# Performance work log

Measured on AMD Instinct MI355X. Metric: run time of the kernel, lower is better.

The kernel has to match this reference:

```python
import jax, jax.numpy as jnp
import numpy as np

E = 768; H = 64; W = 64; K = 3; PAD = 1
CH = [30, 100, 150, 220, 268]


def _conv3x3(x, w, b):
    out = jax.lax.conv_general_dilated(x, w, (1, 1), ((PAD, PAD), (PAD, PAD)),
                                       dimension_numbers=('NCHW', 'OIHW', 'NCHW'))
    return out + b[None, :, None, None]


def _deform_conv(x, offset, mask, w, b):
    # modulated deform_conv2d, group=1, stride=1, dil=1, pad=1 (torchvision semantics)
    N, C, Hh, Ww = x.shape
    KK = K * K
    off = offset.reshape(N, KK, 2, Hh, Ww)  # [...,0]=dy, [...,1]=dx per kernel tap
    ky = jnp.repeat(jnp.arange(K), K).astype(x.dtype)
    kx = jnp.tile(jnp.arange(K), K).astype(x.dtype)
    hg = jnp.arange(Hh, dtype=x.dtype)[None, None, :, None]
    wg = jnp.arange(Ww, dtype=x.dtype)[None, None, None, :]
    py = hg - PAD + ky[None, :, None, None] + off[:, :, 0]  # [N,9,H,W]
    px = wg - PAD + kx[None, :, None, None] + off[:, :, 1]
    y0 = jnp.floor(py); x0 = jnp.floor(px)
    xf = x.reshape(N, C, Hh * Ww)

    def gather(yi, xi):
        valid = ((yi >= 0) & (yi <= Hh - 1) & (xi >= 0) & (xi <= Ww - 1)).astype(x.dtype)
        yc = jnp.clip(yi, 0, Hh - 1).astype(jnp.int32)
        xc = jnp.clip(xi, 0, Ww - 1).astype(jnp.int32)
        idx = (yc * Ww + xc).reshape(N, 1, KK * Hh * Ww)
        g = jnp.take_along_axis(xf, idx, axis=2).reshape(N, C, KK, Hh, Ww)
        return g * valid[:, None]

    wy1 = py - y0; wx1 = px - x0; wy0 = 1.0 - wy1; wx0 = 1.0 - wx1
    samp = (gather(y0, x0) * (wy0 * wx0)[:, None]
            + gather(y0, x0 + 1) * (wy0 * wx1)[:, None]
            + gather(y0 + 1, x0) * (wy1 * wx0)[:, None]
            + gather(y0 + 1, x0 + 1) * (wy1 * wx1)[:, None])
    samp = samp * mask[:, None]  # modulation
    out = jnp.einsum('nckhw,ock->nohw', samp, w.reshape(w.shape[0], C, KK))
    return out + b[None, :, None, None]


def _block(x, conv_w, conv_b, off_w, off_b, msk_w, msk_b, bn_g, bn_b):
    # DefConv2d.forward: conv -> offset/mask linears -> deform conv -> BN(train stats) -> relu
    N, C, Hh, Ww = x.shape
    om = _conv3x3(x, conv_w, conv_b)
    om_hwc = om.transpose(0, 2, 3, 1)
    offset = (om_hwc @ off_w.T + off_b).transpose(0, 3, 1, 2)  # [N,18,H,W]
    mask = jax.nn.softmax(om_hwc @ msk_w.T + msk_b, axis=-1)   # [N,H,W,9]
    mask = mask.reshape(N, K * K, Hh, Ww)  # raw reshape, exactly as torch .reshape (no permute)
    out = _deform_conv(x, offset, mask, conv_w, conv_b)
    mu = out.mean(axis=(0, 2, 3), keepdims=True)
    var = out.var(axis=(0, 2, 3), keepdims=True)
    out = (out - mu) / jnp.sqrt(var + 1e-5) * bn_g[None, :, None, None] + bn_b[None, :, None, None]
    return jax.nn.relu(out)


def _cam(x, chq_w, chv_w, chz_w, ln_g, ln_b, spq_w, spv_w):
    xin = x
    N, C, Hh, Ww = x.shape  # N must be 1 (matches torch reshapes)
    # channel attention
    wv = jnp.einsum('nchw,oc->nohw', x, chv_w).reshape(C // 2, Hh * Ww)
    wq = jax.nn.softmax(jnp.einsum('nchw,oc->nohw', x, chq_w).reshape(Hh * Ww))
    wz = chz_w @ (wv @ wq)  # [C]
    wz = (wz - wz.mean()) / jnp.sqrt(wz.var() + 1e-5) * ln_g + ln_b
    x = jax.nn.sigmoid(wz)[None, :, None, None] * x
    # spatial attention
    wq = jax.nn.softmax(jnp.einsum('nchw,oc->nohw', x, spq_w).max(axis=(2, 3)).reshape(C // 2))
    wv = jnp.einsum('nchw,oc->nohw', x, spv_w).reshape(C // 2, Hh * Ww)
    wz = jax.nn.sigmoid(wq @ wv).reshape(1, 1, Hh, Ww)
    return wz * x + xin


def _forward(x1, x2, x3, x4, x5, conv_w, conv_b, off_w, off_b, msk_w, msk_b, bn_g, bn_b,
             chq_w, chv_w, chz_w, ln_g, ln_b, spq_w, spv_w,
             w1, w2, w3a, w3b, w4a, w4b, w5a, w5b, norm_g, norm_b):
    xper = [t.transpose(0, 3, 1, 2) for t in (x1, x2, x3, x4, x5)]
    blk = lambda t: _block(t, conv_w, conv_b, off_w, off_b, msk_w, msk_b, bn_g, bn_b)
    c1 = lambda t, w: jnp.einsum('nchw,oc->nohw', t, w)
    o1 = c1(blk(xper[0]), w1)
    o2 = c1(blk(xper[1]), w2)
    o3 = c1(blk(xper[2]), w3a) + c1(xper[2], w3b)
    o4 = c1(blk(xper[3]), w4a) + c1(xper[3], w4b)
    o5 = c1(blk(xper[4]), w5a) + c1(xper[4], w5b)
    out = jnp.concatenate((o1, o2, o3, o4, o5), axis=1)  # sum(CH)=768 channels
    out = _cam(out, chq_w, chv_w, chz_w, ln_g, ln_b, spq_w, spv_w)
    out = (out + xper[4]).transpose(0, 2, 3, 1)
    mu = out.mean(-1, keepdims=True)
    var = out.var(-1, keepdims=True)
    return (out - mu) / jnp.sqrt(var + 1e-5) * norm_g + norm_b


def setup_inputs() -> dict:
    key = jax.random.key(0)
    ks = iter(jax.random.split(key, 40))
    rnd = lambda shape, s=0.05: jax.random.normal(next(ks), shape, dtype=jnp.float32) * s
    d = {}
    for i in range(5):
        d[f'x{i+1}'] = jax.random.normal(next(ks), (1, H, W, E), dtype=jnp.float32)
    d['conv_w'] = rnd((E, E, 3, 3), 0.02)
    d['conv_b'] = jnp.zeros((E,), jnp.float32)
    d['off_w'] = rnd((2 * 9, E), 0.01); d['off_b'] = jnp.zeros((18,), jnp.float32)
    d['msk_w'] = rnd((9, E), 0.01); d['msk_b'] = jnp.zeros((9,), jnp.float32)
    d['bn_g'] = jnp.ones((E,), jnp.float32); d['bn_b'] = jnp.zeros((E,), jnp.float32)
    C = sum(CH)  # 768
    d['chq_w'] = rnd((1, C)); d['chv_w'] = rnd((C // 2, C)); d['chz_w'] = rnd((C, C // 2))
    d['ln_g'] = jnp.ones((C,), jnp.float32); d['ln_b'] = jnp.zeros((C,), jnp.float32)
    d['spq_w'] = rnd((C // 2, C)); d['spv_w'] = rnd((C // 2, C))
    d['w1'] = rnd((CH[0], E)); d['w2'] = rnd((CH[1], E))
    d['w3a'] = rnd((CH[2], E)); d['w3b'] = rnd((CH[2], E))
    d['w4a'] = rnd((CH[3], E)); d['w4b'] = rnd((CH[3], E))
    d['w5a'] = rnd((CH[4], E)); d['w5b'] = rnd((CH[4], E))
    d['norm_g'] = jnp.ones((E,), jnp.float32); d['norm_b'] = jnp.zeros((E,), jnp.float32)
    return d


def reference(x1, x2, x3, x4, x5, conv_w, conv_b, off_w, off_b, msk_w, msk_b, bn_g, bn_b,
              chq_w, chv_w, chz_w, ln_g, ln_b, spq_w, spv_w,
              w1, w2, w3a, w3b, w4a, w4b, w5a, w5b, norm_g, norm_b):
    return _forward(x1, x2, x3, x4, x5, conv_w, conv_b, off_w, off_b, msk_w, msk_b, bn_g, bn_b,
                    chq_w, chv_w, chz_w, ln_g, ln_b, spq_w, spv_w,
                    w1, w2, w3a, w3b, w4a, w4b, w5a, w5b, norm_g, norm_b)
```

## Files before the change

kernel.cpp:

```cpp
#include <hip/hip_runtime.h>
#include <cstdint>
#include <cstddef>

#define HW 4096
#define CDIM 768
#define PPIX 4356

typedef unsigned short u16;
typedef __attribute__((ext_vector_type(8))) short short8;
typedef __attribute__((ext_vector_type(4))) float f32x4;

__device__ __forceinline__ float bf2f(u16 u) { return __uint_as_float(((unsigned)u) << 16); }
__device__ __forceinline__ u16 f2bf(float f) {
    unsigned u = __float_as_uint(f);
    unsigned r = (u + 0x7fffu + ((u >> 16) & 1u)) >> 16;
    return (u16)r;
}
__device__ __forceinline__ float lof(unsigned u) { return __uint_as_float(u << 16); }
__device__ __forceinline__ float hif(unsigned u) { return __uint_as_float(u & 0xffff0000u); }
__device__ __forceinline__ int swz(int r) { return ((r >> 1) ^ (r >> 3)) & 3; }

__device__ __forceinline__ void gl16(const u16* g, u16* l) {
    __builtin_amdgcn_global_load_lds(
        (const __attribute__((address_space(1))) unsigned int*)g,
        (__attribute__((address_space(3))) unsigned int*)l, 16, 0, 0);
}

enum GMode { G_CONV = 0, G_PROJ = 2, G_SPAT = 3 };

struct ProjP {
    const u16* b1[5];
    const u16* b2[5];
    int ch[5];
    int choff[5];
};

template <int MODE>
__launch_bounds__(256, 4)
__global__ void k_gemm128(const u16* __restrict__ xpad, const u16* __restrict__ blkA,
                          const u16* __restrict__ Wt, const float* __restrict__ bias,
                          u16* __restrict__ outb, float* __restrict__ outf, ProjP pp) {
    const int z = blockIdx.z;
    const int m0 = blockIdx.x * 128;
    const int n0 = blockIdx.y * 128;

    int Nrows, ntap, choff = 0, ldo = CDIM;
    const u16 *Az = nullptr, *Ac = nullptr, *B1 = nullptr, *B2 = nullptr;
    if constexpr (MODE == G_CONV) {
        Az = xpad + (size_t)z * PPIX * CDIM; B1 = Wt; Nrows = 768; ntap = 9;
    } else if constexpr (MODE == G_PROJ) {
        Ac = blkA + (size_t)z * HW * CDIM;
        Az = xpad + (size_t)z * PPIX * CDIM;
        B1 = pp.b1[z]; B2 = pp.b2[z];
        Nrows = pp.ch[z]; choff = pp.choff[z];
        ntap = B2 ? 2 : 1;
        if (n0 >= Nrows) return;
    } else {
        Ac = blkA; B1 = Wt; Nrows = 384; ntap = 1; ldo = 384;
    }

    __shared__ __align__(16) u16 As[128 * 32];
    __shared__ __align__(16) u16 Bs[128 * 32];

    const int t = threadIdx.x;
    const int lane = t & 63;
    const int wid = t >> 6;
    const int wrow = (wid >> 1) * 64, wcol = (wid & 1) * 64;
    const int lm = lane & 15;
    const int quad = lane >> 4;

    const int rS = t >> 2;
    const int cs0 = (t & 3) ^ swz(rS);
    const int cs1 = (t & 3) ^ swz(64 + rS);

    const u16 *a0 = nullptr, *a1 = nullptr, *a0x = nullptr, *a1x = nullptr;
    if constexpr (MODE == G_CONV) {
        int p0 = m0 + rS, p1 = m0 + 64 + rS;
        a0 = Az + (size_t)(((p0 >> 6)) * 66 + (p0 & 63)) * CDIM + cs0 * 8;
        a1 = Az + (size_t)(((p1 >> 6)) * 66 + (p1 & 63)) * CDIM + cs1 * 8;
    } else if constexpr (MODE == G_PROJ) {
        int p0 = m0 + rS, p1 = m0 + 64 + rS;
        a0 = Ac + (size_t)p0 * CDIM + cs0 * 8;
        a1 = Ac + (size_t)p1 * CDIM + cs1 * 8;
        a0x = Az + (size_t)(((p0 >> 6) + 1) * 66 + (p0 & 63) + 1) * CDIM + cs0 * 8;
        a1x = Az + (size_t)(((p1 >> 6) + 1) * 66 + (p1 & 63) + 1) * CDIM + cs1 * 8;
    } else {
        a0 = Ac + (size_t)(m0 + rS) * CDIM + cs0 * 8;
        a1 = Ac + (size_t)(m0 + 64 + rS) * CDIM + cs1 * 8;
    }
    const u16* b0 = B1 + (size_t)(n0 + rS) * CDIM + cs0 * 8;
    const u16* b1p = B1 + (size_t)(n0 + 64 + rS) * CDIM + cs1 * 8;
    const u16 *c0 = nullptr, *c1 = nullptr;
    if constexpr (MODE == G_PROJ) {
        if (B2) {
            c0 = B2 + (size_t)(n0 + rS) * CDIM + cs0 * 8;
            c1 = B2 + (size_t)(n0 + 64 + rS) * CDIM + cs1 * 8;
        }
    }

    u16* dA0 = &As[(0 * 4 + wid) * 512];
    u16* dA1 = &As[(1 * 4 + wid) * 512];
    u16* dB0 = &Bs[(0 * 4 + wid) * 512];
    u16* dB1 = &Bs[(1 * 4 + wid) * 512];

    f32x4 acc[4][4];
#pragma unroll
    for (int i = 0; i < 4; i++)
#pragma unroll
        for (int j = 0; j < 4; j++) acc[i][j] = (f32x4){0.f, 0.f, 0.f, 0.f};

    const int totS = ntap * 24;
    int tap = 0;
    int tA = 0, tB = 0, kO = 0;

    for (int s = 0; s < totS; ++s) {
        __syncthreads();
        if constexpr (MODE == G_CONV) {
            gl16(a0 + tA + kO, dA0);
            gl16(a1 + tA + kO, dA1);
            gl16(b0 + tB + kO, dB0);
            gl16(b1p + tB + kO, dB1);
        } else if constexpr (MODE == G_PROJ) {
            if (tap == 0) {
                gl16(a0 + kO, dA0);
                gl16(a1 + kO, dA1);
                gl16(b0 + kO, dB0);
                gl16(b1p + kO, dB1);
            } else {
                gl16(a0x + kO, dA0);
                gl16(a1x + kO, dA1);
                gl16(c0 + kO, dB0);
                gl16(c1 + kO, dB1);
            }
        } else {
            gl16(a0 + kO, dA0);
            gl16(a1 + kO, dA1);
            gl16(b0 + kO, dB0);
            gl16(b1p + kO, dB1);
        }
        __syncthreads();
        short8 af[4], bf[4];
#pragma unroll
        for (int i = 0; i < 4; i++) {
            int rr = wrow + i * 16 + lm;
            af[i] = *(const short8*)&As[rr * 32 + ((quad ^ swz(rr)) * 8)];
        }
#pragma unroll
        for (int j = 0; j < 4; j++) {
            int rr = wcol + j * 16 + lm;
            bf[j] = *(const short8*)&Bs[rr * 32 + ((quad ^ swz(rr)) * 8)];
        }
#pragma unroll
        for (int i = 0; i < 4; i++)
#pragma unroll
            for (int j = 0; j < 4; j++)
                acc[i][j] = __builtin_amdgcn_mfma_f32_16x16x32_bf16(af[i], bf[j], acc[i][j], 0, 0, 0);
        tap++;
        if constexpr (MODE == G_CONV) {
            tA += (tap == 3 || tap == 6) ? 64 * CDIM : CDIM;
            tB += CDIM * CDIM;
            if (tap == 9) { tap = 0; tA = 0; tB = 0; kO += 32; }
        } else {
            if (tap == ntap) { tap = 0; kO += 32; }
        }
    }

    if constexpr (MODE == G_CONV) {
        u16* outz = outb + (size_t)z * HW * CDIM;
#pragma unroll
        for (int j = 0; j < 4; j++) {
            int gc = n0 + wcol + j * 16 + lm;
            float bv = bias[gc];
#pragma unroll
            for (int i = 0; i < 4; i++)
#pragma unroll
                for (int r = 0; r < 4; r++) {
                    int gr = m0 + wrow + i * 16 + quad * 4 + r;
                    outz[(size_t)gr * CDIM + gc] = f2bf(acc[i][j][r] + bv);
                }
        }
    } else {
#pragma unroll
        for (int j = 0; j < 4; j++) {
            int gc = n0 + wcol + j * 16 + lm;
            if (gc < Nrows) {
#pragma unroll
                for (int i = 0; i < 4; i++)
#pragma unroll
                    for (int r = 0; r < 4; r++) {
                        int gr = m0 + wrow + i * 16 + quad * 4 + r;
                        outf[(size_t)gr * ldo + choff + gc] = acc[i][j][r];
                    }
            }
        }
    }
}

__launch_bounds__(512, 4)
__global__ void k_conv256(const u16* __restrict__ xpad, const u16* __restrict__ Wt,
                          const float* __restrict__ bias, u16* __restrict__ outb) {
    const int z = blockIdx.z;
    const int m0 = blockIdx.x * 128;
    const int n0 = blockIdx.y * 256;
    const u16* Az = xpad + (size_t)z * PPIX * CDIM;

    __shared__ __align__(16) u16 As[2][128 * 32];
    __shared__ __align__(16) u16 Bs[2][256 * 32];

    const int t = threadIdx.x;
    const int lane = t & 63;
    const int wid = t >> 6;
    const int wrow = (wid >> 2) * 64, wcol = (wid & 3) * 64;
    const int lm = lane & 15;
    const int quad = lane >> 4;

    const int rA = t >> 2;
    const int cA = (t & 3) ^ swz(rA);
    const int rB0 = t >> 2;
    const int cB0 = (t & 3) ^ swz(rB0);
    const int rB1 = 128 + (t >> 2);
    const int cB1 = (t & 3) ^ swz(rB1);

    const int p0 = m0 + rA;
    const u16* aB = Az + (size_t)((p0 >> 6) * 66 + (p0 & 63)) * CDIM + cA * 8;
    const u16* bB0 = Wt + (size_t)(n0 + rB0) * CDIM + cB0 * 8;
    const u16* bB1 = Wt + (size_t)(n0 + rB1) * CDIM + cB1 * 8;

    f32x4 acc[4][4];
#pragma unroll
    for (int i = 0; i < 4; i++)
#pragma unroll
        for (int j = 0; j < 4; j++) acc[i][j] = (f32x4){0.f, 0.f, 0.f, 0.f};

    gl16(aB, &As[0][wid * 512]);
    gl16(bB0, &Bs[0][wid * 512]);
    gl16(bB1, &Bs[0][4096 + wid * 512]);

    int tap = 0, tA = 0, tB = 0, kO = 0;

    for (int s = 0; s < 216; ++s) {
        const int cur = s & 1;
        const int nxt = cur ^ 1;
        __syncthreads();
        const bool hasN = (s + 1 < 216);
        if (hasN) {
            tap++;
            tA += (tap == 3 || tap == 6) ? 64 * CDIM : CDIM;
            tB += CDIM * CDIM;
            if (tap == 9) { tap = 0; tA = 0; tB = 0; kO += 32; }
            gl16(aB + tA + kO, &As[nxt][wid * 512]);
            gl16(bB0 + tB + kO, &Bs[nxt][wid * 512]);
            gl16(bB1 + tB + kO, &Bs[nxt][4096 + wid * 512]);
        }
        short8 af[4];
#pragma unroll
        for (int i = 0; i < 4; i++) {
            int rr = wrow + i * 16 + lm;
            af[i] = *(const short8*)&As[cur][rr * 32 + ((quad ^ swz(rr)) * 8)];
        }
#pragma unroll
        for (int j = 0; j < 4; j++) {
            int rr = wcol + j * 16 + lm;
            short8 bf = *(const short8*)&Bs[cur][rr * 32 + ((quad ^ swz(rr)) * 8)];
#pragma unroll
            for (int i = 0; i < 4; i++)
                acc[i][j] = __builtin_amdgcn_mfma_f32_16x16x32_bf16(af[i], bf, acc[i][j], 0, 0, 0);
        }
    }

    u16* outz = outb + (size_t)z * HW * CDIM;
#pragma unroll
    for (int j = 0; j < 4; j++) {
        int gc = n0 + wcol + j * 16 + lm;
        float bv = bias[gc];
#pragma unroll
        for (int i = 0; i < 4; i++)
#pragma unroll
            for (int r = 0; r < 4; r++) {
                int gr = m0 + wrow + i * 16 + quad * 4 + r;
                outz[(size_t)gr * CDIM + gc] = f2bf(acc[i][j][r] + bv);
            }
    }
}

__launch_bounds__(512, 4)
__global__ void k_gdef(const u16* __restrict__ xpad, const u16* __restrict__ Wt,
                       const int4* __restrict__ idx4, const float4* __restrict__ w4,
                       const float* __restrict__ bias, u16* __restrict__ outb) {
    const int z = blockIdx.z;
    const int m0 = blockIdx.x * 128;
    const int n0 = blockIdx.y * 256;
    const u16* Az = xpad + (size_t)z * PPIX * CDIM;
    const int4* idxz = idx4 + (size_t)z * 9 * 4096;
    const float4* w4z = w4 + (size_t)z * 9 * 4096;

    __shared__ __align__(16) u16 As[2][128 * 32];
    __shared__ __align__(16) u16 Bs[2][256 * 32];

    const int t = threadIdx.x;
    const int lane = t & 63;
    const int wid = t >> 6;
    const int wrow = (wid >> 2) * 64, wcol = (wid & 3) * 64;
    const int lm = lane & 15;
    const int quad = lane >> 4;

    const int rA = t >> 2;
    const int cA = (t & 3) ^ swz(rA);
    const int rB0 = t >> 2;
    const int cB0 = (t & 3) ^ swz(rB0);
    const int rB1 = 128 + (t >> 2);
    const int cB1 = (t & 3) ^ swz(rB1);

    f32x4 acc[4][4];
#pragma unroll
    for (int i = 0; i < 4; i++)
#pragma unroll
        for (int j = 0; j < 4; j++) acc[i][j] = (f32x4){0.f, 0.f, 0.f, 0.f};

    const u16* bP0;
    const u16* bP1;
    int dOff[4];
    float4 wv;

    auto setupSub = [&](int sn) {
        const u16* Bb = Wt + (size_t)sn * CDIM * CDIM;
        bP0 = Bb + (size_t)(n0 + rB0) * CDIM + cB0 * 8;
        bP1 = Bb + (size_t)(n0 + rB1) * CDIM + cB1 * 8;
        int4 iv = idxz[sn * 4096 + m0 + rA];
        wv = w4z[sn * 4096 + m0 + rA];
        dOff[0] = (iv.x + cA * 8) * 2;
        dOff[1] = (iv.y + cA * 8) * 2;
        dOff[2] = (iv.z + cA * 8) * 2;
        dOff[3] = (iv.w + cA * 8) * 2;
    };

    auto blend4 = [&](const uint4* L) -> uint4 {
        auto bl = [&](unsigned a, unsigned b, unsigned c2, unsigned d) -> unsigned {
            float lo = fmaf(wv.x, lof(a), fmaf(wv.y, lof(b), fmaf(wv.z, lof(c2), wv.w * lof(d))));
            float hi = fmaf(wv.x, hif(a), fmaf(wv.y, hif(b), fmaf(wv.z, hif(c2), wv.w * hif(d))));
            return __builtin_amdgcn_perm(__float_as_uint(hi), __float_as_uint(lo), 0x07060302u);
        };
        uint4 o;
        o.x = bl(L[0].x, L[1].x, L[2].x, L[3].x);
        o.y = bl(L[0].y, L[1].y, L[2].y, L[3].y);
        o.z = bl(L[0].z, L[1].z, L[2].z, L[3].z);
        o.w = bl(L[0].w, L[1].w, L[2].w, L[3].w);
        return o;
    };

    setupSub(0);
    int stagedSub = 0;

    {
        uint4 L[4];
#pragma unroll
        for (int k = 0; k < 4; k++)
            L[k] = *(const uint4*)((const char*)Az + dOff[k]);
        gl16(bP0, &Bs[0][wid * 512]);
        gl16(bP1, &Bs[0][4096 + wid * 512]);
        uint4 o = blend4(L);
        *(uint4*)&As[0][t * 8] = o;
    }

    for (int s = 0; s < 216; ++s) {
        const int cur = s & 1;
        const int nxt = cur ^ 1;
        __syncthreads();
        const bool hasN = (s + 1 < 216);
        uint4 L[4];
        if (hasN) {
            int kn = (s + 1) - stagedSub * 24;
            if (kn == 24) { setupSub(++stagedSub); kn = 0; }
            const int cb = kn * 64;
#pragma unroll
            for (int k = 0; k < 4; k++)
                L[k] = *(const uint4*)((const char*)Az + dOff[k] + cb);
            gl16(bP0 + kn * 32, &Bs[nxt][wid * 512]);
            gl16(bP1 + kn * 32, &Bs[nxt][4096 + wid * 512]);
        }
        short8 af[4];
#pragma unroll
        for (int i = 0; i < 4; i++) {
            int rr = wrow + i * 16 + lm;
            af[i] = *(const short8*)&As[cur][rr * 32 + ((quad ^ swz(rr)) * 8)];
        }
#pragma unroll
        for (int j = 0; j < 4; j++) {
            int rr = wcol + j * 16 + lm;
            short8 bf = *(const short8*)&Bs[cur][rr * 32 + ((quad ^ swz(rr)) * 8)];
#pragma unroll
            for (int i = 0; i < 4; i++)
                acc[i][j] = __builtin_amdgcn_mfma_f32_16x16x32_bf16(af[i], bf, acc[i][j], 0, 0, 0);
        }
        if (hasN) {
            uint4 o = blend4(L);
            *(uint4*)&As[nxt][t * 8] = o;
        }
    }

    u16* outz = outb + (size_t)z * HW * CDIM;
#pragma unroll
    for (int j = 0; j < 4; j++) {
        int gc = n0 + wcol + j * 16 + lm;
        float bv = bias[gc];
#pragma unroll
        for (int i = 0; i < 4; i++)
#pragma unroll
            for (int r = 0; r < 4; r++) {
                int gr = m0 + wrow + i * 16 + quad * 4 + r;
                outz[(size_t)gr * CDIM + gc] = f2bf(acc[i][j][r] + bv);
            }
    }
}

struct Ptr5 { const float* p[5]; };

__global__ void k_prep_xpad(Ptr5 xs, u16* __restrict__ xpad) {
    int z = blockIdx.y;
    int pidx = blockIdx.x;
    int ph = pidx / 66, pw = pidx - ph * 66;
    int e0 = threadIdx.x * 4;
    u16* d = xpad + ((size_t)z * PPIX + pidx) * CDIM + e0;
    if (ph == 0 || ph == 65 || pw == 0 || pw == 65) {
        *(uint2*)d = make_uint2(0, 0);
        return;
    }
    const float* s = xs.p[z] + ((size_t)((ph - 1) * 64 + (pw - 1))) * CDIM + e0;
    float4 v = *(const float4*)s;
    u16 o[4] = {f2bf(v.x), f2bf(v.y), f2bf(v.z), f2bf(v.w)};
    *(uint2*)d = *(uint2*)o;
}

__global__ void k_prep_wt(const float* __restrict__ cw, u16* __restrict__ Wt) {
    int o = blockIdx.x;
    for (int c = threadIdx.x; c < 768; c += 256) {
        const float* s = cw + ((size_t)o * 768 + c) * 9;
#pragma unroll
        for (int k = 0; k < 9; k++)
            Wt[(size_t)k * 768 * 768 + (size_t)o * 768 + c] = f2bf(s[k]);
    }
}

struct WbP { const float* src[9]; u16* dst[9]; int n[9]; };

__global__ void k_prep_wb(WbP wp) {
    int m = blockIdx.y;
    int i = (blockIdx.x * 256 + threadIdx.x) * 4;
    if (i >= wp.n[m]) return;
    float4 v = *(const float4*)(wp.src[m] + i);
    u16* d = wp.dst[m] + i;
    d[0] = f2bf(v.x); d[1] = f2bf(v.y); d[2] = f2bf(v.z); d[3] = f2bf(v.w);
}

__global__ void k_offmask1(const u16* __restrict__ om, const float* __restrict__ off_w,
                           const float* __restrict__ off_b, const float* __restrict__ msk_w,
                           const float* __restrict__ msk_b, float* __restrict__ offs,
                           float* __restrict__ msoft) {
    int z = blockIdx.y;
    int wid = threadIdx.x >> 6, lane = threadIdx.x & 63;
    int p = blockIdx.x * 4 + wid;
    const u16* r = om + (size_t)z * HW * CDIM + (size_t)p * CDIM;
    float v[12];
#pragma unroll
    for (int j = 0; j < 12; j++) v[j] = bf2f(r[lane + 64 * j]);
    float lg[9];
#pragma unroll
    for (int qq = 0; qq < 27; qq++) {
        const float* wr = (qq < 18) ? (off_w + qq * 768) : (msk_w + (qq - 18) * 768);
        float s = 0.f;
#pragma unroll
        for (int j = 0; j < 12; j++) s += v[j] * wr[lane + 64 * j];
#pragma unroll
        for (int o = 32; o > 0; o >>= 1) s += __shfl_xor(s, o, 64);
        if (qq < 18) {
            if (lane == qq) offs[((size_t)z * HW + p) * 18 + qq] = s + off_b[qq];
        } else {
            lg[qq - 18] = s + msk_b[qq - 18];
        }
    }
    float mx = -1e30f;
#pragma unroll
    for (int j = 0; j < 9; j++) mx = fmaxf(mx, lg[j]);
    float sum = 0.f;
#pragma unroll
    for (int j = 0; j < 9; j++) { lg[j] = expf(lg[j] - mx); sum += lg[j]; }
    float inv = 1.f / sum;
#pragma unroll
    for (int j = 0; j < 9; j++)
        if (lane == j) msoft[(size_t)z * 36864 + p * 9 + j] = lg[j] * inv;
}

__device__ __forceinline__ int cidx(int y, int x) {
    int yc = min(max(y, 0), 63), xc = min(max(x, 0), 63);
    return ((yc + 1) * 66 + (xc + 1)) * CDIM;
}
__device__ __forceinline__ float cval(int y, int x) {
    return (y >= 0 && y < 64 && x >= 0 && x < 64) ? 1.f : 0.f;
}

__global__ void k_offmask2(const float* __restrict__ offs, const float* __restrict__ msoft,
                           int4* __restrict__ idx4o, float4* __restrict__ w4o) {
    int id = blockIdx.x * 256 + threadIdx.x;
    int z = id / 36864, r = id % 36864, k = r >> 12, p = r & 4095;
    const float* ofz = offs + ((size_t)z * HW + p) * 18;
    float dy = ofz[2 * k], dx = ofz[2 * k + 1];
    float mk = msoft[(size_t)z * 36864 + k * 4096 + p];
    int h = p >> 6, w = p & 63;
    float py = (float)(h - 1 + k / 3) + dy;
    float px = (float)(w - 1 + k % 3) + dx;
    float y0f = floorf(py), x0f = floorf(px);
    int y0 = (int)y0f, x0 = (int)x0f;
    float wy1 = py - y0f, wx1 = px - x0f, wy0 = 1.f - wy1, wx0 = 1.f - wx1;
    idx4o[id] = make_int4(cidx(y0, x0), cidx(y0, x0 + 1), cidx(y0 + 1, x0), cidx(y0 + 1, x0 + 1));
    w4o[id] = make_float4(wy0 * wx0 * cval(y0, x0) * mk, wy0 * wx1 * cval(y0, x0 + 1) * mk,
                          wy1 * wx0 * cval(y0 + 1, x0) * mk, wy1 * wx1 * cval(y0 + 1, x0 + 1) * mk);
}

__global__ void k_bnstats2(const u16* __restrict__ dout, float* __restrict__ pb1,
                           float* __restrict__ pb2) {
    const int z = blockIdx.z, seg = blockIdx.y;
    const int cx = threadIdx.x & 7, py = threadIdx.x >> 3;
    const int c0 = blockIdx.x * 64 + cx * 8;
    const u16* base = dout + (size_t)z * HW * CDIM + (size_t)(seg * 1024) * CDIM + c0;
    float s1[8] = {0.f, 0.f, 0.f, 0.f, 0.f, 0.f, 0.f, 0.f};
    float s2[8] = {0.f, 0.f, 0.f, 0.f, 0.f, 0.f, 0.f, 0.f};
    for (int p = py; p < 1024; p += 32) {
        uint4 v = *(const uint4*)(base + (size_t)p * CDIM);
        const u16* u = (const u16*)&v;
#pragma unroll
        for (int e = 0; e < 8; e++) {
            float f = bf2f(u[e]);
            s1[e] += f; s2[e] += f * f;
        }
    }
    __shared__ float l1[32][64], l2[32][64];
#pragma unroll
    for (int e = 0; e < 8; e++) {
        l1[py][cx * 8 + e] = s1[e];
        l2[py][cx * 8 + e] = s2[e];
    }
    __syncthreads();
    if (threadIdx.x < 64) {
        float a = 0.f, b = 0.f;
        for (int y = 0; y < 32; y++) { a += l1[y][threadIdx.x]; b += l2[y][threadIdx.x]; }
        int ch = blockIdx.x * 64 + threadIdx.x;
        pb1[(z * 4 + seg) * 768 + ch] = a;
        pb2[(z * 4 + seg) * 768 + ch] = b;
    }
}

__global__ void k_bnfinal(const float* __restrict__ pb1, const float* __restrict__ pb2,
                          float* __restrict__ mu, float* __restrict__ rs) {
    int i = blockIdx.x * 256 + threadIdx.x;
    if (i >= 3840) return;
    int z = i / 768, ch = i % 768;
    float a = 0.f, b = 0.f;
#pragma unroll
    for (int s = 0; s < 4; s++) {
        a += pb1[(z * 4 + s) * 768 + ch];
        b += pb2[(z * 4 + s) * 768 + ch];
    }
    float m = a / 4096.f;
    float var = b / 4096.f - m * m;
    mu[i] = m;
    rs[i] = rsqrtf(var + 1e-5f);
}

__global__ void k_bnapply(const u16* __restrict__ dout, const float* __restrict__ mu,
                          const float* __restrict__ rs, const float* __restrict__ g,
                          const float* __restrict__ b, u16* __restrict__ blk) {
    size_t i = ((size_t)blockIdx.x * 256 + threadIdx.x) * 8;
    int c = (int)(i % CDIM);
    int z = (int)(i / ((size_t)HW * CDIM));
    const float* muz = mu + z * 768;
    const float* rsz = rs + z * 768;
    uint4 in = *(const uint4*)(dout + i);
    const u16* u = (const u16*)&in;
    u16 o[8];
#pragma unroll
    for (int e = 0; e < 8; e++) {
        int ce = c + e;
        float v = (bf2f(u[e]) - muz[ce]) * rsz[ce] * g[ce] + b[ce];
        o[e] = f2bf(fmaxf(v, 0.f));
    }
    *(uint4*)(blk + i) = *(uint4*)o;
}

__global__ void k_q(const float* __restrict__ X, const float* __restrict__ chq,
                    float* __restrict__ q) {
    int wid = threadIdx.x >> 6, lane = threadIdx.x & 63;
    int p = blockIdx.x * 4 + wid;
    const float* xr = X + (size_t)p * CDIM;
    float s = 0.f;
#pragma unroll
    for (int j = 0; j < 12; j++) s += xr[lane + 64 * j] * chq[lane + 64 * j];
#pragma unroll
    for (int o = 32; o > 0; o >>= 1) s += __shfl_xor(s, o, 64);
    if (lane == 0) q[p] = s;
}

__global__ void k_soft4096(const float* __restrict__ q, float* __restrict__ sqn,
                           float* __restrict__ xq) {
    __shared__ float red[4];
    int tid = threadIdx.x, lane = tid & 63, wid = tid >> 6;
    float m = -1e30f;
    for (int i = tid; i < 4096; i += 256) m = fmaxf(m, q[i]);
    for (int o = 32; o > 0; o >>= 1) m = fmaxf(m, __shfl_xor(m, o, 64));
    if (lane == 0) red[wid] = m;
    __syncthreads();
    float bm = fmaxf(fmaxf(red[0], red[1]), fmaxf(red[2], red[3]));
    __syncthreads();
    float s = 0.f;
    for (int i = tid; i < 4096; i += 256) {
        float e = expf(q[i] - bm);
        sqn[i] = e; s += e;
    }
    for (int o = 32; o > 0; o >>= 1) s += __shfl_xor(s, o, 64);
    if (lane == 0) red[wid] = s;
    __syncthreads();
    float inv = 1.f / (red[0] + red[1] + red[2] + red[3]);
    for (int i = tid; i < 4096; i += 256) sqn[i] *= inv;
    for (int c = tid; c < 768; c += 256) xq[c] = 0.f;
}

__global__ void k_xq(const float* __restrict__ X, const float* __restrict__ sqn,
                     float* __restrict__ xq) {
    int p0 = blockIdx.x * 128;
    for (int c = threadIdx.x; c < 768; c += 256) {
        float a = 0.f;
        for (int p = p0; p < p0 + 128; p++) a += sqn[p] * X[(size_t)p * CDIM + c];
        atomicAdd(&xq[c], a);
    }
}

__global__ void k_gemv384(const float* __restrict__ chv, const float* __restrict__ xq,
                          float* __restrict__ wvq) {
    int wid = threadIdx.x >> 6, lane = threadIdx.x & 63;
    int o = blockIdx.x * 4 + wid;
    const float* r = chv + (size_t)o * 768;
    float s = 0.f;
#pragma unroll
    for (int j = 0; j < 12; j++) s += r[lane + 64 * j] * xq[lane + 64 * j];
#pragma unroll
    for (int off = 32; off > 0; off >>= 1) s += __shfl_xor(s, off, 64);
    if (lane == 0) wvq[o] = s;
}

__global__ void k_gemv768(const float* __restrict__ chz, const float* __restrict__ wvq,
                          float* __restrict__ wzv) {
    int wid = threadIdx.x >> 6, lane = threadIdx.x & 63;
    int c = blockIdx.x * 4 + wid;
    const float* r = chz + (size_t)c * 384;
    float s = 0.f;
#pragma unroll
    for (int j = 0; j < 6; j++) s += r[lane + 64 * j] * wvq[lane + 64 * j];
#pragma unroll
    for (int off = 32; off > 0; off >>= 1) s += __shfl_xor(s, off, 64);
    if (lane == 0) wzv[c] = s;
}

__global__ void k_lngate(const float* __restrict__ wzv, const float* __restrict__ lng,
                         const float* __restrict__ lnb, float* __restrict__ sgate) {
    __shared__ float red[8];
    int tid = threadIdx.x, lane = tid & 63, wid = tid >> 6;
    float a = wzv[tid], b = wzv[tid + 256], c = wzv[tid + 512];
    float s1 = a + b + c, s2 = a * a + b * b + c * c;
    for (int o = 32; o > 0; o >>= 1) { s1 += __shfl_xor(s1, o, 64); s2 += __shfl_xor(s2, o, 64); }
    if (lane == 0) { red[wid] = s1; red[4 + wid] = s2; }
    __syncthreads();
    s1 = red[0] + red[1] + red[2] + red[3];
    s2 = red[4] + red[5] + red[6] + red[7];
    float mean = s1 / 768.f, var = s2 / 768.f - mean * mean, rstd = rsqrtf(var + 1e-5f);
    for (int cc = tid; cc < 768; cc += 256) {
        float tv = (wzv[cc] - mean) * rstd * lng[cc] + lnb[cc];
        sgate[cc] = 1.f / (1.f + expf(-tv));
    }
}

__global__ void k_xatt(const float* __restrict__ X, const float* __restrict__ sgate,
                       u16* __restrict__ xatt) {
    size_t i = ((size_t)blockIdx.x * 256 + threadIdx.x) * 4;
    int c = (int)(i % CDIM);
    float4 v = *(const float4*)(X + i);
    u16 o[4] = {f2bf(v.x * sgate[c]), f2bf(v.y * sgate[c + 1]),
                f2bf(v.z * sgate[c + 2]), f2bf(v.w * sgate[c + 3])};
    *(uint2*)(xatt + i) = *(uint2*)o;
}

__global__ void k_colmax24(const float* __restrict__ P2, float* __restrict__ m2) {
    __shared__ float red[16][17];
    int col = blockIdx.x * 16 + threadIdx.x;
    float m = -1e30f;
    for (int p = threadIdx.y; p < 4096; p += 16) m = fmaxf(m, P2[(size_t)p * 384 + col]);
    red[threadIdx.y][threadIdx.x] = m;
    __syncthreads();
    if (threadIdx.y == 0) {
        for (int y = 1; y < 16; y++) m = fmaxf(m, red[y][threadIdx.x]);
        m2[col] = m;
    }
}

__global__ void k_sm384(const float* __restrict__ m2, float* __restrict__ sq2) {
    __shared__ float red[6];
    int tid = threadIdx.x, lane = tid & 63, wid = tid >> 6;
    float v = m2[tid];
    float m = v;
    for (int o = 32; o > 0; o >>= 1) m = fmaxf(m, __shfl_xor(m, o, 64));
    if (lane == 0) red[wid] = m;
    __syncthreads();
    m = red[0];
    for (int w = 1; w < 6; w++) m = fmaxf(m, red[w]);
    __syncthreads();
    float e = expf(v - m);
    float s = e;
    for (int o = 32; o > 0; o >>= 1) s += __shfl_xor(s, o, 64);
    if (lane == 0) red[wid] = s;
    __syncthreads();
    float tot = 0.f;
    for (int w = 0; w < 6; w++) tot += red[w];
    sq2[tid] = e / tot;
}

__global__ void k_sv(const float* __restrict__ sq2, const float* __restrict__ spv,
                     float* __restrict__ sv) {
    __shared__ float part[4][64];
    int c = blockIdx.x * 64 + (threadIdx.x & 63);
    int seg = threadIdx.x >> 6;
    float a = 0.f;
    for (int o = seg * 96; o < seg * 96 + 96; o++) a += sq2[o] * spv[(size_t)o * 768 + c];
    part[seg][threadIdx.x & 63] = a;
    __syncthreads();
    if (seg == 0) sv[c] = part[0][threadIdx.x] + part[1][threadIdx.x] +
                          part[2][threadIdx.x] + part[3][threadIdx.x];
}

__global__ void k_final(const float* __restrict__ X, const float* __restrict__ x5,
                        const float* __restrict__ sgate, const float* __restrict__ sv,
                        const float* __restrict__ ng, const float* __restrict__ nb,
                        float* __restrict__ out) {
    int wid = threadIdx.x >> 6, lane = threadIdx.x & 63;
    int p = blockIdx.x * 4 + wid;
    const float* xr = X + (size_t)p * CDIM;
    const float* x5r = x5 + (size_t)p * CDIM;
    float xa[12];
    float d = 0.f;
#pragma unroll
    for (int j = 0; j < 12; j++) {
        int c = lane + 64 * j;
        float a = xr[c] * sgate[c];
        xa[j] = a;
        d += sv[c] * a;
    }
#pragma unroll
    for (int o = 32; o > 0; o >>= 1) d += __shfl_xor(d, o, 64);
    float wz2 = 1.f / (1.f + expf(-d));
    float s1 = 0.f, s2 = 0.f;
#pragma unroll
    for (int j = 0; j < 12; j++) {
        int c = lane + 64 * j;
        float y = wz2 * xa[j] + xr[c] + x5r[c];
        xa[j] = y;
        s1 += y; s2 += y * y;
    }
#pragma unroll
    for (int o = 32; o > 0; o >>= 1) { s1 += __shfl_xor(s1, o, 64); s2 += __shfl_xor(s2, o, 64); }
    float mean = s1 / 768.f, var = s2 / 768.f - mean * mean, rstd = rsqrtf(var + 1e-5f);
#pragma unroll
    for (int j = 0; j < 12; j++) {
        int c = lane + 64 * j;
        out[(size_t)p * CDIM + c] = (xa[j] - mean) * rstd * ng[c] + nb[c];
    }
}

extern "C" void kernel_launch(void* const* d_in, const int* in_sizes, int n_in,
                              void* d_out, int out_size, void* d_ws, size_t ws_size,
                              hipStream_t stream) {
    const float* xin[5];
    for (int i = 0; i < 5; i++) xin[i] = (const float*)d_in[i];
    const float* conv_w = (const float*)d_in[5];
    const float* conv_b = (const float*)d_in[6];
    const float* off_w = (const float*)d_in[7];
    const float* off_b = (const float*)d_in[8];
    const float* msk_w = (const float*)d_in[9];
    const float* msk_b = (const float*)d_in[10];
    const float* bn_g = (const float*)d_in[11];
    const float* bn_b = (const float*)d_in[12];
    const float* chq_w = (const float*)d_in[13];
    const float* chv_w = (const float*)d_in[14];
    const float* chz_w = (const float*)d_in[15];
    const float* ln_g = (const float*)d_in[16];
    const float* ln_b = (const float*)d_in[17];
    const float* spq_w = (const float*)d_in[18];
    const float* spv_w = (const float*)d_in[19];
    const float* wsrc[8];
    for (int i = 0; i < 8; i++) wsrc[i] = (const float*)d_in[20 + i];
    const float* norm_g = (const float*)d_in[28];
    const float* norm_b = (const float*)d_in[29];
    float* out = (float*)d_out;

    char* wsb = (char*)d_ws;
    size_t off = 0;
    auto take = [&](size_t n) -> char* {
        char* p = wsb + off;
        off = (off + n + 255) & ~(size_t)255;
        return p;
    };
    u16* xpad = (u16*)take(5ll * PPIX * CDIM * 2);
    u16* Wt = (u16*)take(9ll * CDIM * CDIM * 2);
    u16* omblk = (u16*)take(5ll * HW * CDIM * 2);
    float* offs = (float*)take(5ll * HW * 18 * 4);
    float* msoft = (float*)take(5ll * 36864 * 4);
    int4* idx4 = (int4*)take(5ll * 9 * 4096 * 16);
    float4* w4 = (float4*)take(5ll * 9 * 4096 * 16);
    u16* dout = (u16*)take(5ll * HW * CDIM * 2);
    u16* wb = (u16*)take(1790ll * 768 * 2);
    float* Xcat = (float*)take((size_t)HW * CDIM * 4);
    float* mu = (float*)take(5 * 768 * 4);
    float* rs = (float*)take(5 * 768 * 4);
    float* pb1 = (float*)take(5 * 4 * 768 * 4);
    float* pb2 = (float*)take(5 * 4 * 768 * 4);
    float* qv = (float*)take(4096 * 4);
    float* sqn = (float*)take(4096 * 4);
    float* xq = (float*)take(768 * 4);
    float* wvq = (float*)take(384 * 4);
    float* wzv = (float*)take(768 * 4);
    float* sgate = (float*)take(768 * 4);
    float* m2 = (float*)take(384 * 4);
    float* sq2 = (float*)take(384 * 4);
    float* sv = (float*)take(768 * 4);
    u16* xatt = dout;
    float* P2 = (float*)((char*)dout + 8388608);
    u16* blk = omblk;
    (void)ws_size; (void)in_sizes; (void)n_in; (void)out_size;

    int rows[9] = {30, 100, 150, 150, 220, 220, 268, 268, 384};
    int roff[9]; int acc = 0;
    for (int i = 0; i < 9; i++) { roff[i] = acc; acc += rows[i]; }
    u16* spqb = wb + (size_t)roff[8] * 768;

    WbP wp;
    for (int i = 0; i < 8; i++) { wp.src[i] = wsrc[i]; wp.dst[i] = wb + (size_t)roff[i] * 768; wp.n[i] = rows[i] * 768; }
    wp.src[8] = spq_w; wp.dst[8] = spqb; wp.n[8] = rows[8] * 768;

    ProjP pp;
    pp.b1[0] = wb + (size_t)roff[0] * 768; pp.b2[0] = nullptr;
    pp.b1[1] = wb + (size_t)roff[1] * 768; pp.b2[1] = nullptr;
    pp.b1[2] = wb + (size_t)roff[2] * 768; pp.b2[2] = wb + (size_t)roff[3] * 768;
    pp.b1[3] = wb + (size_t)roff[4] * 768; pp.b2[3] = wb + (size_t)roff[5] * 768;
    pp.b1[4] = wb + (size_t)roff[6] * 768; pp.b2[4] = wb + (size_t)roff[7] * 768;
    int chs[5] = {30, 100, 150, 220, 268};
    int cof[5] = {0, 30, 130, 280, 500};
    for (int i = 0; i < 5; i++) { pp.ch[i] = chs[i]; pp.choff[i] = cof[i]; }
    ProjP pdum = {};

    Ptr5 xs;
    for (int i = 0; i < 5; i++) xs.p[i] = xin[i];

    k_prep_xpad<<<dim3(PPIX, 5), 192, 0, stream>>>(xs, xpad);
    k_prep_wt<<<dim3(768), 256, 0, stream>>>(conv_w, Wt);
    k_prep_wb<<<dim3(288, 9), 256, 0, stream>>>(wp);

    k_conv256<<<dim3(32, 3, 5), 512, 0, stream>>>(xpad, Wt, conv_b, omblk);
    k_offmask1<<<dim3(1024, 5), 256, 0, stream>>>(omblk, off_w, off_b, msk_w, msk_b, offs, msoft);
    k_offmask2<<<dim3(720), 256, 0, stream>>>(offs, msoft, idx4, w4);
    k_gdef<<<dim3(32, 3, 5), 512, 0, stream>>>(xpad, Wt, idx4, w4, conv_b, dout);
    k_bnstats2<<<dim3(12, 4, 5), 256, 0, stream>>>(dout, pb1, pb2);
    k_bnfinal<<<dim3(15), 256, 0, stream>>>(pb1, pb2, mu, rs);
    k_bnapply<<<dim3(7680), 256, 0, stream>>>(dout, mu, rs, bn_g, bn_b, blk);
    k_gemm128<G_PROJ><<<dim3(32, 3, 5), 256, 0, stream>>>(xpad, blk, nullptr, nullptr,
                                                          nullptr, Xcat, pp);

    k_q<<<dim3(1024), 256, 0, stream>>>(Xcat, chq_w, qv);
    k_soft4096<<<dim3(1), 256, 0, stream>>>(qv, sqn, xq);
    k_xq<<<dim3(32), 256, 0, stream>>>(Xcat, sqn, xq);
    k_gemv384<<<dim3(96), 256, 0, stream>>>(chv_w, xq, wvq);
    k_gemv768<<<dim3(192), 256, 0, stream>>>(chz_w, wvq, wzv);
    k_lngate<<<dim3(1), 256, 0, stream>>>(wzv, ln_g, ln_b, sgate);
    k_xatt<<<dim3(3072), 256, 0, stream>>>(Xcat, sgate, xatt);
    k_gemm128<G_SPAT><<<dim3(32, 3, 1), 256, 0, stream>>>(xpad, xatt, spqb, nullptr,
                                                          nullptr, P2, pdum);
    k_colmax24<<<dim3(24), dim3(16, 16), 0, stream>>>(P2, m2);
    k_sm384<<<dim3(1), 384, 0, stream>>>(m2, sq2);
    k_sv<<<dim3(12), 256, 0, stream>>>(sq2, spv_w, sv);

    k_final<<<dim3(1024), 256, 0, stream>>>(Xcat, xin[4], sgate, sv, norm_g, norm_b, out);
}
```

Before: 996.3 us.

## Fold offset/mask linears into conv weights and swizzle deform GEMM blocks per XCD

The 3x3 conv producing the 768-channel intermediate is used only through the 27 offset/mask linear projections. So the linear weights are folded into the conv weights (a 9x32x768 bf16 matrix plus a folded bias), and a narrow 32-column conv GEMM now writes the offsets and mask logits directly. This removes the full 768x768x9 conv GEMM, the bf16 intermediate buffer write, and the separate offmask1 pass; the softmax moves into offmask2. It also remaps k_gdef block indices so that consecutive work lands on the same XCD, for better L2 reuse. The folded weights are rounded to bf16 and the intermediate is no longer rounded to bf16, which changes numerics slightly.

```diff
diff --git a/kernel.cpp b/kernel.cpp
--- a/kernel.cpp
+++ b/kernel.cpp
@@ -196,90 +196,131 @@
     }
 }
 
+__device__ __forceinline__ void xcd_decode(int bid, int& m0, int& n0, int& z) {
+    int work = (bid & 7) * 60 + (bid >> 3);
+    z = work / 96;
+    int rem = work - z * 96;
+    n0 = (rem >> 5) * 256;
+    m0 = (rem & 31) * 128;
+}
+
+__global__ void k_fold(const u16* __restrict__ Wt, const float* __restrict__ off_w,
+                       const float* __restrict__ msk_w, u16* __restrict__ OMW) {
+    const int cb = blockIdx.x, tp = blockIdx.y, qg = blockIdx.z;
+    const int q0 = qg * 9;
+    __shared__ float ow[256 * 9];
+    const int c = cb * 256 + threadIdx.x;
+    const u16* wcol = Wt + (size_t)tp * 768 * 768 + c;
+    float acc[9];
+#pragma unroll
+    for (int qi = 0; qi < 9; qi++) acc[qi] = 0.f;
+    for (int ob = 0; ob < 768; ob += 256) {
+        __syncthreads();
+#pragma unroll
+        for (int qi = 0; qi < 9; qi++) {
+            int q = q0 + qi;
+            const float* src = (q < 18) ? (off_w + (size_t)q * 768)
+                                        : (msk_w + (size_t)(q - 18) * 768);
+            ow[threadIdx.x * 9 + qi] = src[ob + threadIdx.x];
+        }
+        __syncthreads();
+#pragma unroll 4
+        for (int oo = 0; oo < 256; oo++) {
+            float w = bf2f(wcol[(size_t)(ob + oo) * 768]);
+#pragma unroll
+            for (int qi = 0; qi < 9; qi++) acc[qi] = fmaf(w, ow[oo * 9 + qi], acc[qi]);
+        }
+    }
+#pragma unroll
+    for (int qi = 0; qi < 9; qi++)
+        OMW[((size_t)tp * 32 + q0 + qi) * 768 + c] = f2bf(acc[qi]);
+    if (qg == 2) {
+        for (int q = 27; q < 32; q++) OMW[((size_t)tp * 32 + q) * 768 + c] = 0;
+    }
+}
+
+__global__ void k_bias27(const float* __restrict__ off_w, const float* __restrict__ msk_w,
+                         const float* __restrict__ conv_b, const float* __restrict__ off_b,
+                         const float* __restrict__ msk_b, float* __restrict__ bb) {
+    int wid = threadIdx.x >> 6, lane = threadIdx.x & 63;
+    int q = blockIdx.x * 4 + wid;
+    if (q >= 27) return;
+    const float* r = (q < 18) ? (off_w + (size_t)q * 768) : (msk_w + (size_t)(q - 18) * 768);
+    float s = 0.f;
+#pragma unroll
+    for (int j = 0; j < 12; j++) s += r[lane + 64 * j] * conv_b[lane + 64 * j];
+#pragma unroll
+    for (int o = 32; o > 0; o >>= 1) s += __shfl_xor(s, o, 64);
+    if (lane == 0) bb[q] = s + ((q < 18) ? off_b[q] : msk_b[q - 18]);
+}
+
 __launch_bounds__(512, 4)
-__global__ void k_conv256(const u16* __restrict__ xpad, const u16* __restrict__ Wt,
-                          const float* __restrict__ bias, u16* __restrict__ outb) {
+__global__ void k_convOM(const u16* __restrict__ xpad, const u16* __restrict__ OMW,
+                         const float* __restrict__ bb, float* __restrict__ offs,
+                         float* __restrict__ mlog) {
     const int z = blockIdx.z;
     const int m0 = blockIdx.x * 128;
-    const int n0 = blockIdx.y * 256;
     const u16* Az = xpad + (size_t)z * PPIX * CDIM;
 
     __shared__ __align__(16) u16 As[2][128 * 32];
-    __shared__ __align__(16) u16 Bs[2][256 * 32];
+    __shared__ __align__(16) u16 Bs[2][32 * 32];
 
     const int t = threadIdx.x;
     const int lane = t & 63;
     const int wid = t >> 6;
-    const int wrow = (wid >> 2) * 64, wcol = (wid & 3) * 64;
     const int lm = lane & 15;
     const int quad = lane >> 4;
 
     const int rA = t >> 2;
     const int cA = (t & 3) ^ swz(rA);
-    const int rB0 = t >> 2;
-    const int cB0 = (t & 3) ^ swz(rB0);
-    const int rB1 = 128 + (t >> 2);
-    const int cB1 = (t & 3) ^ swz(rB1);
-
     const int p0 = m0 + rA;
     const u16* aB = Az + (size_t)((p0 >> 6) * 66 + (p0 & 63)) * CDIM + cA * 8;
-    const u16* bB0 = Wt + (size_t)(n0 + rB0) * CDIM + cB0 * 8;
-    const u16* bB1 = Wt + (size_t)(n0 + rB1) * CDIM + cB1 * 8;
-
-    f32x4 acc[4][4];
-#pragma unroll
-    for (int i = 0; i < 4; i++)
-#pragma unroll
-        for (int j = 0; j < 4; j++) acc[i][j] = (f32x4){0.f, 0.f, 0.f, 0.f};
+
+    const int rB = t >> 2;
+    const int cB = (t & 3) ^ swz(rB);
+    const u16* bB = OMW + (size_t)rB * 768 + cB * 8;
+
+    f32x4 acc[2];
+    acc[0] = (f32x4){0.f, 0.f, 0.f, 0.f};
+    acc[1] = (f32x4){0.f, 0.f, 0.f, 0.f};
 
     gl16(aB, &As[0][wid * 512]);
-    gl16(bB0, &Bs[0][wid * 512]);
-    gl16(bB1, &Bs[0][4096 + wid * 512]);
+    if (t < 128) gl16(bB, &Bs[0][wid * 512]);
 
     int tap = 0, tA = 0, tB = 0, kO = 0;
-
     for (int s = 0; s < 216; ++s) {
-        const int cur = s & 1;
-        const int nxt = cur ^ 1;
+        const int cur = s & 1, nxt = cur ^ 1;
         __syncthreads();
         const bool hasN = (s + 1 < 216);
         if (hasN) {
             tap++;
             tA += (tap == 3 || tap == 6) ? 64 * CDIM : CDIM;
-            tB += CDIM * CDIM;
+            tB += 32 * 768;
             if (tap == 9) { tap = 0; tA = 0; tB = 0; kO += 32; }
             gl16(aB + tA + kO, &As[nxt][wid * 512]);
-            gl16(bB0 + tB + kO, &Bs[nxt][wid * 512]);
-            gl16(bB1 + tB + kO, &Bs[nxt][4096 + wid * 512]);
-        }
-        short8 af[4];
-#pragma unroll
-        for (int i = 0; i < 4; i++) {
-            int rr = wrow + i * 16 + lm;
-            af[i] = *(const short8*)&As[cur][rr * 32 + ((quad ^ swz(rr)) * 8)];
-        }
-#pragma unroll
-        for (int j = 0; j < 4; j++) {
-            int rr = wcol + j * 16 + lm;
+            if (t < 128) gl16(bB + tB + kO, &Bs[nxt][wid * 512]);
+        }
+        int ar = wid * 16 + lm;
+        short8 af = *(const short8*)&As[cur][ar * 32 + ((quad ^ swz(ar)) * 8)];
+#pragma unroll
+        for (int j = 0; j < 2; j++) {
+            int rr = j * 16 + lm;
             short8 bf = *(const short8*)&Bs[cur][rr * 32 + ((quad ^ swz(rr)) * 8)];
-#pragma unroll
-            for (int i = 0; i < 4; i++)
-                acc[i][j] = __builtin_amdgcn_mfma_f32_16x16x32_bf16(af[i], bf, acc[i][j], 0, 0, 0);
-        }
-    }
-
-    u16* outz = outb + (size_t)z * HW * CDIM;
-#pragma unroll
-    for (int j = 0; j < 4; j++) {
-        int gc = n0 + wcol + j * 16 + lm;
-        float bv = bias[gc];
-#pragma unroll
-        for (int i = 0; i < 4; i++)
-#pragma unroll
-            for (int r = 0; r < 4; r++) {
-                int gr = m0 + wrow + i * 16 + quad * 4 + r;
-                outz[(size_t)gr * CDIM + gc] = f2bf(acc[i][j][r] + bv);
-            }
+            acc[j] = __builtin_amdgcn_mfma_f32_16x16x32_bf16(af, bf, acc[j], 0, 0, 0);
+        }
+    }
+
+#pragma unroll
+    for (int j = 0; j < 2; j++) {
+        int gc = j * 16 + lm;
+        float bv = (gc < 27) ? bb[gc] : 0.f;
+#pragma unroll
+        for (int r = 0; r < 4; r++) {
+            int gr = m0 + wid * 16 + quad * 4 + r;
+            float v = acc[j][r] + bv;
+            if (gc < 18) offs[((size_t)z * HW + gr) * 18 + gc] = v;
+            else if (gc < 27) mlog[(size_t)z * 36864 + (size_t)gr * 9 + (gc - 18)] = v;
+        }
     }
 }
 
@@ -287,9 +328,8 @@
 __global__ void k_gdef(const u16* __restrict__ xpad, const u16* __restrict__ Wt,
                        const int4* __restrict__ idx4, const float4* __restrict__ w4,
                        const float* __restrict__ bias, u16* __restrict__ outb) {
-    const int z = blockIdx.z;
-    const int m0 = blockIdx.x * 128;
-    const int n0 = blockIdx.y * 256;
+    int m0, n0, z;
+    xcd_decode(blockIdx.x, m0, n0, z);
     const u16* Az = xpad + (size_t)z * PPIX * CDIM;
     const int4* idxz = idx4 + (size_t)z * 9 * 4096;
     const float4* w4z = w4 + (size_t)z * 9 * 4096;
@@ -452,44 +492,6 @@
     d[0] = f2bf(v.x); d[1] = f2bf(v.y); d[2] = f2bf(v.z); d[3] = f2bf(v.w);
 }
 
-__global__ void k_offmask1(const u16* __restrict__ om, const float* __restrict__ off_w,
-                           const float* __restrict__ off_b, const float* __restrict__ msk_w,
-                           const float* __restrict__ msk_b, float* __restrict__ offs,
-                           float* __restrict__ msoft) {
-    int z = blockIdx.y;
-    int wid = threadIdx.x >> 6, lane = threadIdx.x & 63;
-    int p = blockIdx.x * 4 + wid;
-    const u16* r = om + (size_t)z * HW * CDIM + (size_t)p * CDIM;
-    float v[12];
-#pragma unroll
-    for (int j = 0; j < 12; j++) v[j] = bf2f(r[lane + 64 * j]);
-    float lg[9];
-#pragma unroll
-    for (int qq = 0; qq < 27; qq++) {
-        const float* wr = (qq < 18) ? (off_w + qq * 768) : (msk_w + (qq - 18) * 768);
-        float s = 0.f;
-#pragma unroll
-        for (int j = 0; j < 12; j++) s += v[j] * wr[lane + 64 * j];
-#pragma unroll
-        for (int o = 32; o > 0; o >>= 1) s += __shfl_xor(s, o, 64);
-        if (qq < 18) {
-            if (lane == qq) offs[((size_t)z * HW + p) * 18 + qq] = s + off_b[qq];
-        } else {
-            lg[qq - 18] = s + msk_b[qq - 18];
-        }
-    }
-    float mx = -1e30f;
-#pragma unroll
-    for (int j = 0; j < 9; j++) mx = fmaxf(mx, lg[j]);
-    float sum = 0.f;
-#pragma unroll
-    for (int j = 0; j < 9; j++) { lg[j] = expf(lg[j] - mx); sum += lg[j]; }
-    float inv = 1.f / sum;
-#pragma unroll
-    for (int j = 0; j < 9; j++)
-        if (lane == j) msoft[(size_t)z * 36864 + p * 9 + j] = lg[j] * inv;
-}
-
 __device__ __forceinline__ int cidx(int y, int x) {
     int yc = min(max(y, 0), 63), xc = min(max(x, 0), 63);
     return ((yc + 1) * 66 + (xc + 1)) * CDIM;
@@ -498,13 +500,22 @@
     return (y >= 0 && y < 64 && x >= 0 && x < 64) ? 1.f : 0.f;
 }
 
-__global__ void k_offmask2(const float* __restrict__ offs, const float* __restrict__ msoft,
+__global__ void k_offmask2(const float* __restrict__ offs, const float* __restrict__ mlog,
                            int4* __restrict__ idx4o, float4* __restrict__ w4o) {
     int id = blockIdx.x * 256 + threadIdx.x;
     int z = id / 36864, r = id % 36864, k = r >> 12, p = r & 4095;
     const float* ofz = offs + ((size_t)z * HW + p) * 18;
     float dy = ofz[2 * k], dx = ofz[2 * k + 1];
-    float mk = msoft[(size_t)z * 36864 + k * 4096 + p];
+    int flat = k * 4096 + p;
+    int P = flat / 9, jj = flat - P * 9;
+    const float* ml = mlog + (size_t)z * 36864 + (size_t)P * 9;
+    float l[9], mx = -1e30f;
+#pragma unroll
+    for (int i2 = 0; i2 < 9; i2++) { l[i2] = ml[i2]; mx = fmaxf(mx, l[i2]); }
+    float sum = 0.f;
+#pragma unroll
+    for (int i2 = 0; i2 < 9; i2++) sum += expf(l[i2] - mx);
+    float mk = expf(l[jj] - mx) / sum;
     int h = p >> 6, w = p & 63;
     float py = (float)(h - 1 + k / 3) + dy;
     float px = (float)(w - 1 + k % 3) + dx;
@@ -809,11 +820,13 @@
     u16* Wt = (u16*)take(9ll * CDIM * CDIM * 2);
     u16* omblk = (u16*)take(5ll * HW * CDIM * 2);
     float* offs = (float*)take(5ll * HW * 18 * 4);
-    float* msoft = (float*)take(5ll * 36864 * 4);
+    float* mlog = (float*)take(5ll * 36864 * 4);
     int4* idx4 = (int4*)take(5ll * 9 * 4096 * 16);
     float4* w4 = (float4*)take(5ll * 9 * 4096 * 16);
     u16* dout = (u16*)take(5ll * HW * CDIM * 2);
     u16* wb = (u16*)take(1790ll * 768 * 2);
+    u16* OMW = (u16*)take(9ll * 32 * 768 * 2);
+    float* bb = (float*)take(32 * 4);
     float* Xcat = (float*)take((size_t)HW * CDIM * 4);
     float* mu = (float*)take(5 * 768 * 4);
     float* rs = (float*)take(5 * 768 * 4);
@@ -859,11 +872,12 @@
     k_prep_xpad<<<dim3(PPIX, 5), 192, 0, stream>>>(xs, xpad);
     k_prep_wt<<<dim3(768), 256, 0, stream>>>(conv_w, Wt);
     k_prep_wb<<<dim3(288, 9), 256, 0, stream>>>(wp);
-
-    k_conv256<<<dim3(32, 3, 5), 512, 0, stream>>>(xpad, Wt, conv_b, omblk);
-    k_offmask1<<<dim3(1024, 5), 256, 0, stream>>>(omblk, off_w, off_b, msk_w, msk_b, offs, msoft);
-    k_offmask2<<<dim3(720), 256, 0, stream>>>(offs, msoft, idx4, w4);
-    k_gdef<<<dim3(32, 3, 5), 512, 0, stream>>>(xpad, Wt, idx4, w4, conv_b, dout);
+    k_fold<<<dim3(3, 9, 3), 256, 0, stream>>>(Wt, off_w, msk_w, OMW);
+    k_bias27<<<dim3(7), 256, 0, stream>>>(off_w, msk_w, conv_b, off_b, msk_b, bb);
+
+    k_convOM<<<dim3(32, 1, 5), 512, 0, stream>>>(xpad, OMW, bb, offs, mlog);
+    k_offmask2<<<dim3(720), 256, 0, stream>>>(offs, mlog, idx4, w4);
+    k_gdef<<<dim3(480), 512, 0, stream>>>(xpad, Wt, idx4, w4, conv_b, dout);
     k_bnstats2<<<dim3(12, 4, 5), 256, 0, stream>>>(dout, pb1, pb2);
     k_bnfinal<<<dim3(15), 256, 0, stream>>>(pb1, pb2, mu, rs);
     k_bnapply<<<dim3(7680), 256, 0, stream>>>(dout, mu, rs, bn_g, bn_b, blk);
```

Result: faster. 859.8 us (-13.7%).
